# Performance work log

Hardware: AMD Instinct MI355X
Metric: run time of the kernel (lower is better)

Reference implementation:

```python
import jax, jax.numpy as jnp
import numpy as np

D_MODEL, H, D_FF = 1024, 16, 4096
B, S = 2, 2048
EPS = 1e-6


def setup_inputs() -> dict:
    key = jax.random.key(0)
    ks = jax.random.split(key, 12)
    sc = 0.02
    p = lambda k, shape: (jax.random.normal(k, shape, dtype=jnp.float32) * sc)
    return {
        "x": jax.random.normal(ks[0], (B, S, D_MODEL), dtype=jnp.float32),
        "mask": jnp.ones((B, 1, 1, S), dtype=jnp.int32),
        "wq": p(ks[1], (D_MODEL, D_MODEL)), "bq": jnp.zeros((D_MODEL,), jnp.float32),
        "wk": p(ks[2], (D_MODEL, D_MODEL)), "bk": jnp.zeros((D_MODEL,), jnp.float32),
        "wv": p(ks[3], (D_MODEL, D_MODEL)), "bv": jnp.zeros((D_MODEL,), jnp.float32),
        "wo": p(ks[4], (D_MODEL, D_MODEL)), "bo": jnp.zeros((D_MODEL,), jnp.float32),
        "w1": p(ks[5], (D_FF, D_MODEL)), "b1": jnp.zeros((D_FF,), jnp.float32),
        "w2": p(ks[6], (D_MODEL, D_FF)), "b2": jnp.zeros((D_MODEL,), jnp.float32),
        "ln1_a": jnp.ones((D_MODEL,), jnp.float32), "ln1_b": jnp.zeros((D_MODEL,), jnp.float32),
        "ln2_a": jnp.ones((D_MODEL,), jnp.float32), "ln2_b": jnp.zeros((D_MODEL,), jnp.float32),
    }


def _layernorm(x, alpha, beta):
    # Matches the torch module: unbiased std (ddof=1), eps added to std (not var).
    mean = jnp.mean(x, axis=-1, keepdims=True)
    std = jnp.std(x, axis=-1, keepdims=True, ddof=1)
    return alpha * (x - mean) / (std + EPS) + beta


def _mha(x, mask, wq, bq, wk, bk, wv, bv, wo, bo):
    b, s, d = x.shape
    d_k = d // H
    # torch Linear: y = x @ W^T + b
    q = (x @ wq.T + bq).reshape(b, s, H, d_k).transpose(0, 2, 1, 3)
    k = (x @ wk.T + bk).reshape(b, s, H, d_k).transpose(0, 2, 1, 3)
    v = (x @ wv.T + bv).reshape(b, s, H, d_k).transpose(0, 2, 1, 3)
    scores = jnp.einsum("bhqd,bhkd->bhqk", q, k) / jnp.sqrt(jnp.float32(d_k))
    scores = jnp.where(mask == 0, jnp.float32(-1e9), scores)
    attn = jax.nn.softmax(scores, axis=-1)
    out = jnp.einsum("bhqk,bhkd->bhqd", attn, v)
    out = out.transpose(0, 2, 1, 3).reshape(b, s, d)
    return out @ wo.T + bo


def reference(x, mask, wq, bq, wk, bk, wv, bv, wo, bo, w1, b1, w2, b2,
              ln1_a, ln1_b, ln2_a, ln2_b):
    # Pre-LN MHA + residual
    h1 = _layernorm(x, ln1_a, ln1_b)
    x = x + _mha(h1, mask, wq, bq, wk, bk, wv, bv, wo, bo)
    # Pre-LN FFN + residual (dropout=0 -> identity)
    h2 = _layernorm(x, ln2_a, ln2_b)
    ff = jax.nn.relu(h2 @ w1.T + b1) @ w2.T + b2
    return x + ff
```

## Files before the change

kernel.cpp:

```cpp
#include <hip/hip_runtime.h>
#include <cstdint>
#include <cstddef>

typedef short bf16x8 __attribute__((ext_vector_type(8)));
typedef float f32x4 __attribute__((ext_vector_type(4)));

#define D_MODEL 1024
#define SEQ     2048
#define NBATCH  2
#define NH      16
#define DKH     64
#define DFF     4096
#define MROWS   (NBATCH * SEQ)

__device__ __forceinline__ unsigned short f2bf(float f) {
  unsigned u = __builtin_bit_cast(unsigned, f);
  u += 0x7fffu + ((u >> 16) & 1u);
  return (unsigned short)(u >> 16);
}
__device__ __forceinline__ unsigned packbf2(float lo, float hi) {
  unsigned r;
  asm("v_cvt_pk_bf16_f32 %0, %1, %2" : "=v"(r) : "v"(lo), "v"(hi));
  return r;
}
__device__ __forceinline__ void gload_lds16(const void* g, void* l) {
  __builtin_amdgcn_global_load_lds(
      (const __attribute__((address_space(1))) unsigned*)g,
      (__attribute__((address_space(3))) unsigned*)l, 16, 0, 0);
}

__global__ __launch_bounds__(256) void cast_weights_kernel(
    const float* __restrict__ wq, const float* __restrict__ wk,
    const float* __restrict__ wv, const float* __restrict__ wo,
    const float* __restrict__ w1, const float* __restrict__ w2,
    unsigned short* __restrict__ dst) {
  const int TOT4 = (12 << 20) >> 2;
  for (int i4 = blockIdx.x * blockDim.x + threadIdx.x; i4 < TOT4;
       i4 += gridDim.x * blockDim.x) {
    int i = i4 << 2;
    const float* src;
    int off;
    if (i < (4 << 20)) {
      src = (i < (2 << 20)) ? ((i < (1 << 20)) ? wq : wk)
                            : ((i < (3 << 20)) ? wv : wo);
      off = i & ((1 << 20) - 1);
    } else if (i < (8 << 20)) { src = w1; off = i - (4 << 20); }
    else                      { src = w2; off = i - (8 << 20); }
    float4 v = *(const float4*)(src + off);
    ushort4 o;
    o.x = f2bf(v.x); o.y = f2bf(v.y); o.z = f2bf(v.z); o.w = f2bf(v.w);
    *(ushort4*)(dst + i) = o;
  }
}

__global__ __launch_bounds__(256) void ln_kernel(
    const float* __restrict__ x, const float* __restrict__ alpha,
    const float* __restrict__ beta, unsigned short* __restrict__ out) {
  const int row = blockIdx.x;
  const int t = threadIdx.x;
  float4 v = *(const float4*)(x + (size_t)row * D_MODEL + t * 4);
  float s = v.x + v.y + v.z + v.w;
#pragma unroll
  for (int o = 1; o < 64; o <<= 1) s += __shfl_xor(s, o, 64);
  __shared__ float red[8];
  if ((t & 63) == 0) red[t >> 6] = s;
  __syncthreads();
  float mean = (red[0] + red[1] + red[2] + red[3]) * (1.f / D_MODEL);
  float dx = v.x - mean, dy = v.y - mean, dz = v.z - mean, dw = v.w - mean;
  float sq = dx * dx + dy * dy + dz * dz + dw * dw;
#pragma unroll
  for (int o = 1; o < 64; o <<= 1) sq += __shfl_xor(sq, o, 64);
  if ((t & 63) == 0) red[4 + (t >> 6)] = sq;
  __syncthreads();
  float var = (red[4] + red[5] + red[6] + red[7]) * (1.f / (D_MODEL - 1));
  float inv = 1.f / (sqrtf(var) + 1e-6f);
  float4 a = *(const float4*)(alpha + t * 4);
  float4 be = *(const float4*)(beta + t * 4);
  ushort4 o4;
  o4.x = f2bf(a.x * dx * inv + be.x);
  o4.y = f2bf(a.y * dy * inv + be.y);
  o4.z = f2bf(a.z * dz * inv + be.z);
  o4.w = f2bf(a.w * dw * inv + be.w);
  *(ushort4*)(out + (size_t)row * D_MODEL + t * 4) = o4;
}

#define GEMM_STAGE(A_, W_, LD_, koff_, kt_, buf_)                                  \
  {                                                                                \
    int ke_ = (koff_) + (kt_) * 32;                                                \
    gload_lds16(A_ + (size_t)(m0 + srow) * (LD_) + ke_ + sce, &lds[(buf_)][0][t * 8]);        \
    gload_lds16(A_ + (size_t)(m0 + 64 + srow) * (LD_) + ke_ + sce, &lds[(buf_)][0][2048 + t * 8]); \
    gload_lds16(W_ + (size_t)(n0 + srow) * (LD_) + ke_ + sce, &lds[(buf_)][1][t * 8]);        \
    gload_lds16(W_ + (size_t)(n0 + 64 + srow) * (LD_) + ke_ + sce, &lds[(buf_)][1][2048 + t * 8]); \
  }

#define GEMM_MAINLOOP(A_, W_, LD_, K_, koff_)                                      \
  GEMM_STAGE(A_, W_, LD_, koff_, 0, 0);                                            \
  for (int kt = 0; kt < ((K_) >> 5); ++kt) {                                       \
    __syncthreads();                                                               \
    if (kt + 1 < ((K_) >> 5)) GEMM_STAGE(A_, W_, LD_, koff_, kt + 1, (kt + 1) & 1); \
    const unsigned short* la = lds[kt & 1][0];                                     \
    const unsigned short* lb = lds[kt & 1][1];                                     \
    bf16x8 af[4], bfr[4];                                                          \
    _Pragma("unroll") for (int i = 0; i < 4; i++) {                                \
      af[i]  = *(const bf16x8*)&la[(wm + i * 16 + c) * 32 + g * 8];                \
      bfr[i] = *(const bf16x8*)&lb[(wn + i * 16 + c) * 32 + g * 8];                \
    }                                                                              \
    _Pragma("unroll") for (int mi = 0; mi < 4; mi++)                               \
      _Pragma("unroll") for (int ni = 0; ni < 4; ni++)                             \
        acc[mi][ni] = __builtin_amdgcn_mfma_f32_16x16x32_bf16(af[mi], bfr[ni],     \
                                                              acc[mi][ni], 0, 0, 0); \
  }

enum { MODE_BF16 = 0, MODE_RELU = 2, MODE_PARTIAL = 4 };

template <int MODE>
__global__ __launch_bounds__(256) void gemm_bt(
    const unsigned short* __restrict__ A, const unsigned short* __restrict__ W,
    const float* __restrict__ bias, void* __restrict__ outp, int M, int N, int K) {
  __shared__ unsigned short lds[2][2][128 * 32];
  const int t = threadIdx.x;
  const int lane = t & 63, wid = t >> 6;
  const int g = lane >> 4, c = lane & 15;
  const int m0 = blockIdx.y * 128, n0 = blockIdx.x * 128;
  const int wm = (wid >> 1) * 64, wn = (wid & 1) * 64;
  const int srow = t >> 2, sce = (t & 3) * 8;
  const int ldk = K * gridDim.z;
  const int koff = blockIdx.z * K;

  f32x4 zero = {0.f, 0.f, 0.f, 0.f};
  f32x4 acc[4][4];
#pragma unroll
  for (int i = 0; i < 4; i++)
#pragma unroll
    for (int j = 0; j < 4; j++) acc[i][j] = zero;

  GEMM_MAINLOOP(A, W, ldk, K, koff);

  float bv[4];
#pragma unroll
  for (int ni = 0; ni < 4; ni++)
    bv[ni] = (MODE == MODE_PARTIAL) ? 0.f : bias[n0 + wn + ni * 16 + c];

  float* po = (MODE == MODE_PARTIAL)
                  ? ((float*)outp + (size_t)blockIdx.z * M * N) : (float*)outp;

#pragma unroll
  for (int mi = 0; mi < 4; mi++) {
#pragma unroll
    for (int ni = 0; ni < 4; ni++) {
      const int mb = m0 + wm + mi * 16 + g * 4;
      const int n = n0 + wn + ni * 16 + c;
#pragma unroll
      for (int r = 0; r < 4; r++) {
        const int m = mb + r;
        float v = acc[mi][ni][r] + bv[ni];
        if (MODE == MODE_RELU) v = fmaxf(v, 0.f);
        if (MODE == MODE_PARTIAL) {
          po[(size_t)m * N + n] = v;
        } else {
          ((unsigned short*)outp)[(size_t)m * N + n] = f2bf(v);
        }
      }
    }
  }
}

__global__ __launch_bounds__(256) void gemm_qkv(
    const unsigned short* __restrict__ A, const unsigned short* __restrict__ Wbase,
    const float* __restrict__ bq, const float* __restrict__ bk,
    const float* __restrict__ bv_, unsigned short* __restrict__ qkout,
    unsigned short* __restrict__ vtout) {
  __shared__ unsigned short lds[2][2][128 * 32];
  const int t = threadIdx.x;
  const int lane = t & 63, wid = t >> 6;
  const int g = lane >> 4, c = lane & 15;
  const int wsel = blockIdx.x >> 3;
  const int m0 = blockIdx.y * 128, n0 = (blockIdx.x & 7) * 128;
  const int wm = (wid >> 1) * 64, wn = (wid & 1) * 64;
  const int srow = t >> 2, sce = (t & 3) * 8;
  const unsigned short* W = Wbase + ((size_t)wsel << 20);
  const float* bias = (wsel == 0) ? bq : (wsel == 1) ? bk : bv_;

  f32x4 zero = {0.f, 0.f, 0.f, 0.f};
  f32x4 acc[4][4];
#pragma unroll
  for (int i = 0; i < 4; i++)
#pragma unroll
    for (int j = 0; j < 4; j++) acc[i][j] = zero;

  GEMM_MAINLOOP(A, W, 1024, 1024, 0);

  float bvv[4];
#pragma unroll
  for (int ni = 0; ni < 4; ni++) bvv[ni] = bias[n0 + wn + ni * 16 + c];
  const float qsc = (wsel == 0) ? 0.125f : 1.f;

  if (wsel < 2) {
    unsigned short* outp = qkout + ((size_t)wsel << 22);
#pragma unroll
    for (int mi = 0; mi < 4; mi++) {
#pragma unroll
      for (int ni = 0; ni < 4; ni++) {
        const int mb = m0 + wm + mi * 16 + g * 4;
        const int n = n0 + wn + ni * 16 + c;
#pragma unroll
        for (int r = 0; r < 4; r++)
          outp[(size_t)(mb + r) * 1024 + n] = f2bf((acc[mi][ni][r] + bvv[ni]) * qsc);
      }
    }
  } else {
#pragma unroll
    for (int mi = 0; mi < 4; mi++) {
#pragma unroll
      for (int ni = 0; ni < 4; ni++) {
        const int mb = m0 + wm + mi * 16 + g * 4;
        const int n = n0 + wn + ni * 16 + c;
        const int b = mb >> 11, s2 = mb & 2047;
        ushort4 o4;
        o4.x = f2bf(acc[mi][ni][0] + bvv[ni]);
        o4.y = f2bf(acc[mi][ni][1] + bvv[ni]);
        o4.z = f2bf(acc[mi][ni][2] + bvv[ni]);
        o4.w = f2bf(acc[mi][ni][3] + bvv[ni]);
        *(ushort4*)(vtout + ((size_t)(b * 1024 + n)) * 2048 + s2) = o4;
      }
    }
  }
}

#define ATTN_STAGE(base_, buf_)                                                    \
  {                                                                                \
    gload_lds16(Kb + (size_t)((base_) + kr) * D_MODEL + ((kc ^ (kr & 7)) << 3),    \
                &Klds[buf_][t * 8]);                                               \
    gload_lds16(Vb + (size_t)vr * SEQ + (base_) + ((vc2 ^ (vr & 3)) << 3),         \
                &Vlds[buf_][t * 8]);                                               \
  }

__global__ __launch_bounds__(256, 4) void attn_kernel(
    const unsigned short* __restrict__ Q, const unsigned short* __restrict__ Kmat,
    const unsigned short* __restrict__ Vt, const int* __restrict__ mask,
    unsigned short* __restrict__ O) {
  __shared__ unsigned short Klds[2][32 * 64];
  __shared__ unsigned short Vlds[2][64 * 32];
  const int t = threadIdx.x, lane = t & 63, wid = t >> 6;
  const int g = lane >> 4, c = lane & 15;
  const int qt = blockIdx.x, bh = blockIdx.y;
  const int b = bh >> 4, h = bh & 15;
  const int q0 = qt * 64 + wid * 16;

  const unsigned short* Qb = Q + (size_t)b * SEQ * D_MODEL + h * DKH;
  const unsigned short* Kb = Kmat + (size_t)b * SEQ * D_MODEL + h * DKH;
  const unsigned short* Vb = Vt + (size_t)bh * DKH * SEQ;
  const int* mb = mask + b * SEQ;

  const int kr = t >> 3, kc = t & 7;
  const int vr = t >> 2, vc2 = t & 3;

  bf16x8 qf[2];
#pragma unroll
  for (int kd = 0; kd < 2; kd++)
    qf[kd] = *(const bf16x8*)&Qb[(size_t)(q0 + c) * D_MODEL + kd * 32 + g * 8];

  f32x4 zero = {0.f, 0.f, 0.f, 0.f};
  f32x4 of[4];
#pragma unroll
  for (int j = 0; j < 4; j++) of[j] = zero;
  float mrun = -1e30f, lrun = 0.f;

  ATTN_STAGE(0, 0);

  for (int kv = 0; kv < 64; ++kv) {
    const int buf = kv & 1;
    const int base = kv * 32;
    __syncthreads();
    if (kv < 63) ATTN_STAGE(base + 32, buf ^ 1);

    bf16x8 kf[4];
#pragma unroll
    for (int nb = 0; nb < 2; nb++)
#pragma unroll
      for (int kd = 0; kd < 2; kd++)
        kf[nb * 2 + kd] = *(const bf16x8*)&Klds[buf][(nb * 16 + c) * 64 +
                                                     (((kd * 4 + g) ^ (c & 7)) << 3)];
    bf16x8 vf[4];
#pragma unroll
    for (int dkb = 0; dkb < 4; dkb++)
      vf[dkb] = *(const bf16x8*)&Vlds[buf][(dkb * 16 + c) * 32 +
                                           ((g ^ (c & 3)) << 3)];

    int4 mk0 = *(const int4*)&mb[base + g * 4];
    int4 mk1 = *(const int4*)&mb[base + 16 + g * 4];

    f32x4 sf[2];
#pragma unroll
    for (int nb = 0; nb < 2; nb++) {
      f32x4 s = zero;
      s = __builtin_amdgcn_mfma_f32_16x16x32_bf16(kf[nb * 2 + 0], qf[0], s, 0, 0, 0);
      s = __builtin_amdgcn_mfma_f32_16x16x32_bf16(kf[nb * 2 + 1], qf[1], s, 0, 0, 0);
      sf[nb] = s;
    }

    sf[0][0] += (mk0.x == 0) ? -1e9f : 0.f;
    sf[0][1] += (mk0.y == 0) ? -1e9f : 0.f;
    sf[0][2] += (mk0.z == 0) ? -1e9f : 0.f;
    sf[0][3] += (mk0.w == 0) ? -1e9f : 0.f;
    sf[1][0] += (mk1.x == 0) ? -1e9f : 0.f;
    sf[1][1] += (mk1.y == 0) ? -1e9f : 0.f;
    sf[1][2] += (mk1.z == 0) ? -1e9f : 0.f;
    sf[1][3] += (mk1.w == 0) ? -1e9f : 0.f;

    float pm = fmaxf(fmaxf(fmaxf(sf[0][0], sf[0][1]), fmaxf(sf[0][2], sf[0][3])),
                     fmaxf(fmaxf(sf[1][0], sf[1][1]), fmaxf(sf[1][2], sf[1][3])));
    pm = fmaxf(pm, __shfl_xor(pm, 16, 64));
    pm = fmaxf(pm, __shfl_xor(pm, 32, 64));
    if (!__all(pm <= mrun + 8.f)) {
      float mnew = fmaxf(mrun, pm);
      float fsc = exp2f((mrun - mnew) * 1.44269504f);
      lrun *= fsc;
#pragma unroll
      for (int dkb = 0; dkb < 4; dkb++) of[dkb] *= fsc;
      mrun = mnew;
    }
    const float mb2 = mrun * 1.44269504f;
    float ps = 0.f;
#pragma unroll
    for (int nb = 0; nb < 2; nb++)
#pragma unroll
      for (int r = 0; r < 4; r++) {
        float p = exp2f(fmaf(sf[nb][r], 1.44269504f, -mb2));
        sf[nb][r] = p;
        ps += p;
      }
    lrun += ps;

    unsigned pk00 = packbf2(sf[0][0], sf[0][1]);
    unsigned pk01 = packbf2(sf[0][2], sf[0][3]);
    unsigned pk10 = packbf2(sf[1][0], sf[1][1]);
    unsigned pk11 = packbf2(sf[1][2], sf[1][3]);
    const int la = ((g & 1) << 5) + c;
    const int lb2 = la + 16;
    unsigned a00 = __shfl(pk00, la, 64), a01 = __shfl(pk01, la, 64);
    unsigned a10 = __shfl(pk10, la, 64), a11 = __shfl(pk11, la, 64);
    unsigned b00 = __shfl(pk00, lb2, 64), b01 = __shfl(pk01, lb2, 64);
    unsigned b10 = __shfl(pk10, lb2, 64), b11 = __shfl(pk11, lb2, 64);
    const bool hi2 = (g >= 2);
    uint4 pw;
    pw.x = hi2 ? a10 : a00;
    pw.y = hi2 ? a11 : a01;
    pw.z = hi2 ? b10 : b00;
    pw.w = hi2 ? b11 : b01;
    bf16x8 pf = __builtin_bit_cast(bf16x8, pw);
#pragma unroll
    for (int dkb = 0; dkb < 4; dkb++)
      of[dkb] = __builtin_amdgcn_mfma_f32_16x16x32_bf16(vf[dkb], pf, of[dkb], 0, 0, 0);
  }

  float lt = lrun;
  lt += __shfl_xor(lt, 16, 64);
  lt += __shfl_xor(lt, 32, 64);
  float inv = 1.f / lt;
#pragma unroll
  for (int dkb = 0; dkb < 4; dkb++) {
    ushort4 o4;
    o4.x = f2bf(of[dkb][0] * inv);
    o4.y = f2bf(of[dkb][1] * inv);
    o4.z = f2bf(of[dkb][2] * inv);
    o4.w = f2bf(of[dkb][3] * inv);
    *(ushort4*)&O[(size_t)(b * SEQ + q0 + c) * D_MODEL + h * DKH + dkb * 16 +
                  g * 4] = o4;
  }
}

__global__ __launch_bounds__(256) void proj_ln2_kernel(
    const float* __restrict__ x, const float* __restrict__ P0,
    const float* __restrict__ P1, const float* __restrict__ bo,
    const float* __restrict__ alpha, const float* __restrict__ beta,
    float* __restrict__ x2, unsigned short* __restrict__ h2) {
  const int row = blockIdx.x;
  const int t = threadIdx.x;
  const size_t idx = (size_t)row * D_MODEL + t * 4;
  float4 xv = *(const float4*)(x + idx);
  float4 p0 = *(const float4*)(P0 + idx);
  float4 p1 = *(const float4*)(P1 + idx);
  float4 bo4 = *(const float4*)(bo + t * 4);
  float4 v;
  v.x = xv.x + p0.x + p1.x + bo4.x;
  v.y = xv.y + p0.y + p1.y + bo4.y;
  v.z = xv.z + p0.z + p1.z + bo4.z;
  v.w = xv.w + p0.w + p1.w + bo4.w;
  *(float4*)(x2 + idx) = v;

  float s = v.x + v.y + v.z + v.w;
#pragma unroll
  for (int o = 1; o < 64; o <<= 1) s += __shfl_xor(s, o, 64);
  __shared__ float red[8];
  if ((t & 63) == 0) red[t >> 6] = s;
  __syncthreads();
  float mean = (red[0] + red[1] + red[2] + red[3]) * (1.f / D_MODEL);
  float dx = v.x - mean, dy = v.y - mean, dz = v.z - mean, dw = v.w - mean;
  float sq = dx * dx + dy * dy + dz * dz + dw * dw;
#pragma unroll
  for (int o = 1; o < 64; o <<= 1) sq += __shfl_xor(sq, o, 64);
  if ((t & 63) == 0) red[4 + (t >> 6)] = sq;
  __syncthreads();
  float var = (red[4] + red[5] + red[6] + red[7]) * (1.f / (D_MODEL - 1));
  float inv = 1.f / (sqrtf(var) + 1e-6f);
  float4 a = *(const float4*)(alpha + t * 4);
  float4 be = *(const float4*)(beta + t * 4);
  ushort4 o4;
  o4.x = f2bf(a.x * dx * inv + be.x);
  o4.y = f2bf(a.y * dy * inv + be.y);
  o4.z = f2bf(a.z * dz * inv + be.z);
  o4.w = f2bf(a.w * dw * inv + be.w);
  *(ushort4*)(h2 + idx) = o4;
}

__global__ __launch_bounds__(256) void ffn2_add_kernel(
    const float* __restrict__ x2, const float* __restrict__ Q0,
    const float* __restrict__ Q1, const float* __restrict__ b2,
    float* __restrict__ out) {
  const int i4 = blockIdx.x * blockDim.x + threadIdx.x;
  const size_t idx = (size_t)i4 * 4;
  float4 a = *(const float4*)(x2 + idx);
  float4 q0 = *(const float4*)(Q0 + idx);
  float4 q1 = *(const float4*)(Q1 + idx);
  float4 b = *(const float4*)(b2 + ((i4 & 255) * 4));
  float4 v;
  v.x = a.x + q0.x + q1.x + b.x;
  v.y = a.y + q0.y + q1.y + b.y;
  v.z = a.z + q0.z + q1.z + b.z;
  v.w = a.w + q0.w + q1.w + b.w;
  *(float4*)(out + idx) = v;
}

extern "C" void kernel_launch(void* const* d_in, const int* in_sizes, int n_in,
                              void* d_out, int out_size, void* d_ws, size_t ws_size,
                              hipStream_t stream) {
  (void)in_sizes; (void)n_in; (void)out_size; (void)ws_size;
  const float* x    = (const float*)d_in[0];
  const int*   mask = (const int*)d_in[1];
  const float* wq   = (const float*)d_in[2];
  const float* bq   = (const float*)d_in[3];
  const float* wk   = (const float*)d_in[4];
  const float* bk   = (const float*)d_in[5];
  const float* wv   = (const float*)d_in[6];
  const float* bv   = (const float*)d_in[7];
  const float* wo   = (const float*)d_in[8];
  const float* bo   = (const float*)d_in[9];
  const float* w1   = (const float*)d_in[10];
  const float* b1   = (const float*)d_in[11];
  const float* w2   = (const float*)d_in[12];
  const float* b2   = (const float*)d_in[13];
  const float* ln1a = (const float*)d_in[14];
  const float* ln1b = (const float*)d_in[15];
  const float* ln2a = (const float*)d_in[16];
  const float* ln2b = (const float*)d_in[17];

  char* ws = (char*)d_ws;
  unsigned short* w_bf  = (unsigned short*)ws;
  unsigned short* wq_bf = w_bf;
  unsigned short* wo_bf = w_bf + (3u << 20);
  unsigned short* w1_bf = w_bf + (4u << 20);
  unsigned short* w2_bf = w_bf + (8u << 20);
  unsigned short* h1    = (unsigned short*)(ws + (24u << 20));
  unsigned short* qbuf  = (unsigned short*)(ws + (32u << 20));
  unsigned short* kbuf  = (unsigned short*)(ws + (40u << 20));
  unsigned short* vtbuf = (unsigned short*)(ws + (48u << 20));
  unsigned short* attnb = (unsigned short*)(ws + (56u << 20));
  float*          x2    = (float*)(ws + (64u << 20));
  unsigned short* h2    = (unsigned short*)(ws + (80u << 20));
  unsigned short* ffn1  = (unsigned short*)(ws + (88u << 20));
  float*          pp    = (float*)(ws + (88u << 20));
  float*          qq    = (float*)(ws + (24u << 20));

  cast_weights_kernel<<<1024, 256, 0, stream>>>(wq, wk, wv, wo, w1, w2, w_bf);
  ln_kernel<<<MROWS, 256, 0, stream>>>(x, ln1a, ln1b, h1);
  gemm_qkv<<<dim3(24, 32), 256, 0, stream>>>(h1, wq_bf, bq, bk, bv, qbuf, vtbuf);
  attn_kernel<<<dim3(32, 32), 256, 0, stream>>>(qbuf, kbuf, vtbuf, mask, attnb);
  gemm_bt<MODE_PARTIAL><<<dim3(8, 32, 2), 256, 0, stream>>>(
      attnb, wo_bf, nullptr, (void*)pp, MROWS, D_MODEL, 512);
  proj_ln2_kernel<<<MROWS, 256, 0, stream>>>(
      x, pp, pp + (size_t)MROWS * D_MODEL, bo, ln2a, ln2b, x2, h2);
  gemm_bt<MODE_RELU><<<dim3(32, 32), 256, 0, stream>>>(
      h2, w1_bf, b1, (void*)ffn1, MROWS, DFF, D_MODEL);
  gemm_bt<MODE_PARTIAL><<<dim3(8, 32, 2), 256, 0, stream>>>(
      ffn1, w2_bf, nullptr, (void*)qq, MROWS, D_MODEL, 2048);
  ffn2_add_kernel<<<4096, 256, 0, stream>>>(
      x2, qq, qq + (size_t)MROWS * D_MODEL, b2, (float*)d_out);
}
```

Baseline: 297.3 us.

## Shrink attention blocks to two waves and use 16x16x16 MFMA for PV

The attention kernel now runs 128-thread blocks covering 32 query rows, doubling the grid, and each thread issues two LDS-direct loads per K and V tile. The PV product uses 16x16x16 bf16 MFMAs fed directly from the softmax registers, which removes the cross-lane shuffles that repacked P for the 16x16x32 instruction. The int mask is precomputed into an additive float bias inside the weight-cast kernel, so the inner loop adds it instead of doing compares. In exchange, the smaller blocks mean each K/V tile is loaded into LDS by more blocks, and the PV step issues twice as many smaller MFMAs.

```diff
diff --git a/kernel.cpp b/kernel.cpp
--- a/kernel.cpp
+++ b/kernel.cpp
@@ -3,6 +3,7 @@
 #include <cstddef>
 
 typedef short bf16x8 __attribute__((ext_vector_type(8)));
+typedef short bf16x4 __attribute__((ext_vector_type(4)));
 typedef float f32x4 __attribute__((ext_vector_type(4)));
 
 #define D_MODEL 1024
@@ -13,6 +14,16 @@
 #define DFF     4096
 #define MROWS   (NBATCH * SEQ)
 
+#if __has_builtin(__builtin_amdgcn_mfma_f32_16x16x16bf16_1k)
+#define HAVE_MFMA16 1
+#define MFMA16(a, b, c) __builtin_amdgcn_mfma_f32_16x16x16bf16_1k(a, b, c, 0, 0, 0)
+#elif __has_builtin(__builtin_amdgcn_mfma_f32_16x16x16_bf16)
+#define HAVE_MFMA16 1
+#define MFMA16(a, b, c) __builtin_amdgcn_mfma_f32_16x16x16_bf16(a, b, c, 0, 0, 0)
+#else
+#define HAVE_MFMA16 0
+#endif
+
 __device__ __forceinline__ unsigned short f2bf(float f) {
   unsigned u = __builtin_bit_cast(unsigned, f);
   u += 0x7fffu + ((u >> 16) & 1u);
@@ -33,10 +44,11 @@
     const float* __restrict__ wq, const float* __restrict__ wk,
     const float* __restrict__ wv, const float* __restrict__ wo,
     const float* __restrict__ w1, const float* __restrict__ w2,
-    unsigned short* __restrict__ dst) {
+    const int* __restrict__ mask, unsigned short* __restrict__ dst,
+    float* __restrict__ maskf) {
   const int TOT4 = (12 << 20) >> 2;
-  for (int i4 = blockIdx.x * blockDim.x + threadIdx.x; i4 < TOT4;
-       i4 += gridDim.x * blockDim.x) {
+  const int gid = blockIdx.x * blockDim.x + threadIdx.x;
+  for (int i4 = gid; i4 < TOT4; i4 += gridDim.x * blockDim.x) {
     int i = i4 << 2;
     const float* src;
     int off;
@@ -50,6 +62,15 @@
     ushort4 o;
     o.x = f2bf(v.x); o.y = f2bf(v.y); o.z = f2bf(v.z); o.w = f2bf(v.w);
     *(ushort4*)(dst + i) = o;
+  }
+  if (gid < (NBATCH * SEQ / 4)) {
+    int4 m = ((const int4*)mask)[gid];
+    float4 f;
+    f.x = (m.x == 0) ? -1e9f : 0.f;
+    f.y = (m.y == 0) ? -1e9f : 0.f;
+    f.z = (m.z == 0) ? -1e9f : 0.f;
+    f.w = (m.w == 0) ? -1e9f : 0.f;
+    ((float4*)maskf)[gid] = f;
   }
 }
 
@@ -227,17 +248,22 @@
   }
 }
 
-#define ATTN_STAGE(base_, buf_)                                                    \
-  {                                                                                \
-    gload_lds16(Kb + (size_t)((base_) + kr) * D_MODEL + ((kc ^ (kr & 7)) << 3),    \
-                &Klds[buf_][t * 8]);                                               \
-    gload_lds16(Vb + (size_t)vr * SEQ + (base_) + ((vc2 ^ (vr & 3)) << 3),         \
-                &Vlds[buf_][t * 8]);                                               \
-  }
-
-__global__ __launch_bounds__(256, 4) void attn_kernel(
+#define ATTN_STAGE(base_, buf_)                                                     \
+  {                                                                                 \
+    const int i0 = t, i1 = t + 128;                                                 \
+    gload_lds16(Kb + (size_t)((base_) + (i0 >> 3)) * D_MODEL +                      \
+                    (((i0 & 7) ^ ((i0 >> 3) & 7)) << 3), &Klds[buf_][i0 * 8]);      \
+    gload_lds16(Kb + (size_t)((base_) + (i1 >> 3)) * D_MODEL +                      \
+                    (((i1 & 7) ^ ((i1 >> 3) & 7)) << 3), &Klds[buf_][i1 * 8]);      \
+    gload_lds16(Vb + (size_t)(i0 >> 2) * SEQ + (base_) +                            \
+                    (((i0 & 3) ^ ((i0 >> 2) & 3)) << 3), &Vlds[buf_][i0 * 8]);      \
+    gload_lds16(Vb + (size_t)(i1 >> 2) * SEQ + (base_) +                            \
+                    (((i1 & 3) ^ ((i1 >> 2) & 3)) << 3), &Vlds[buf_][i1 * 8]);      \
+  }
+
+__global__ __launch_bounds__(128, 4) void attn_kernel(
     const unsigned short* __restrict__ Q, const unsigned short* __restrict__ Kmat,
-    const unsigned short* __restrict__ Vt, const int* __restrict__ mask,
+    const unsigned short* __restrict__ Vt, const float* __restrict__ maskf,
     unsigned short* __restrict__ O) {
   __shared__ unsigned short Klds[2][32 * 64];
   __shared__ unsigned short Vlds[2][64 * 32];
@@ -245,15 +271,12 @@
   const int g = lane >> 4, c = lane & 15;
   const int qt = blockIdx.x, bh = blockIdx.y;
   const int b = bh >> 4, h = bh & 15;
-  const int q0 = qt * 64 + wid * 16;
+  const int q0 = qt * 32 + wid * 16;
 
   const unsigned short* Qb = Q + (size_t)b * SEQ * D_MODEL + h * DKH;
   const unsigned short* Kb = Kmat + (size_t)b * SEQ * D_MODEL + h * DKH;
   const unsigned short* Vb = Vt + (size_t)bh * DKH * SEQ;
-  const int* mb = mask + b * SEQ;
-
-  const int kr = t >> 3, kc = t & 7;
-  const int vr = t >> 2, vc2 = t & 3;
+  const float* mbf = maskf + b * SEQ;
 
   bf16x8 qf[2];
 #pragma unroll
@@ -281,14 +304,27 @@
       for (int kd = 0; kd < 2; kd++)
         kf[nb * 2 + kd] = *(const bf16x8*)&Klds[buf][(nb * 16 + c) * 64 +
                                                      (((kd * 4 + g) ^ (c & 7)) << 3)];
+#if HAVE_MFMA16
+    bf16x4 vv[2][4];
+#pragma unroll
+    for (int nb = 0; nb < 2; nb++)
+#pragma unroll
+      for (int dkb = 0; dkb < 4; dkb++) {
+        const int vrow = dkb * 16 + c;
+        const int vbyte = vrow * 64 + ((((nb << 1) + (g >> 1)) ^ (c & 3)) << 4) +
+                          ((g & 1) << 3);
+        vv[nb][dkb] = *(const bf16x4*)((const char*)Vlds[buf] + vbyte);
+      }
+#else
     bf16x8 vf[4];
 #pragma unroll
     for (int dkb = 0; dkb < 4; dkb++)
       vf[dkb] = *(const bf16x8*)&Vlds[buf][(dkb * 16 + c) * 32 +
                                            ((g ^ (c & 3)) << 3)];
-
-    int4 mk0 = *(const int4*)&mb[base + g * 4];
-    int4 mk1 = *(const int4*)&mb[base + 16 + g * 4];
+#endif
+
+    float4 ma0 = *(const float4*)&mbf[base + g * 4];
+    float4 ma1 = *(const float4*)&mbf[base + 16 + g * 4];
 
     f32x4 sf[2];
 #pragma unroll
@@ -299,14 +335,8 @@
       sf[nb] = s;
     }
 
-    sf[0][0] += (mk0.x == 0) ? -1e9f : 0.f;
-    sf[0][1] += (mk0.y == 0) ? -1e9f : 0.f;
-    sf[0][2] += (mk0.z == 0) ? -1e9f : 0.f;
-    sf[0][3] += (mk0.w == 0) ? -1e9f : 0.f;
-    sf[1][0] += (mk1.x == 0) ? -1e9f : 0.f;
-    sf[1][1] += (mk1.y == 0) ? -1e9f : 0.f;
-    sf[1][2] += (mk1.z == 0) ? -1e9f : 0.f;
-    sf[1][3] += (mk1.w == 0) ? -1e9f : 0.f;
+    sf[0][0] += ma0.x; sf[0][1] += ma0.y; sf[0][2] += ma0.z; sf[0][3] += ma0.w;
+    sf[1][0] += ma1.x; sf[1][1] += ma1.y; sf[1][2] += ma1.z; sf[1][3] += ma1.w;
 
     float pm = fmaxf(fmaxf(fmaxf(sf[0][0], sf[0][1]), fmaxf(sf[0][2], sf[0][3])),
                      fmaxf(fmaxf(sf[1][0], sf[1][1]), fmaxf(sf[1][2], sf[1][3])));
@@ -332,6 +362,19 @@
       }
     lrun += ps;
 
+#if HAVE_MFMA16
+#pragma unroll
+    for (int nb = 0; nb < 2; nb++) {
+      unsigned plo = packbf2(sf[nb][0], sf[nb][1]);
+      unsigned phi = packbf2(sf[nb][2], sf[nb][3]);
+      unsigned long long uu = (unsigned long long)plo |
+                              ((unsigned long long)phi << 32);
+      bf16x4 pf = __builtin_bit_cast(bf16x4, uu);
+#pragma unroll
+      for (int dkb = 0; dkb < 4; dkb++)
+        of[dkb] = MFMA16(vv[nb][dkb], pf, of[dkb]);
+    }
+#else
     unsigned pk00 = packbf2(sf[0][0], sf[0][1]);
     unsigned pk01 = packbf2(sf[0][2], sf[0][3]);
     unsigned pk10 = packbf2(sf[1][0], sf[1][1]);
@@ -352,6 +395,7 @@
 #pragma unroll
     for (int dkb = 0; dkb < 4; dkb++)
       of[dkb] = __builtin_amdgcn_mfma_f32_16x16x32_bf16(vf[dkb], pf, of[dkb], 0, 0, 0);
+#endif
   }
 
   float lt = lrun;
@@ -471,11 +515,13 @@
   unsigned short* ffn1  = (unsigned short*)(ws + (88u << 20));
   float*          pp    = (float*)(ws + (88u << 20));
   float*          qq    = (float*)(ws + (24u << 20));
-
-  cast_weights_kernel<<<1024, 256, 0, stream>>>(wq, wk, wv, wo, w1, w2, w_bf);
+  float*          maskf = (float*)(ws + (120u << 20));
+
+  cast_weights_kernel<<<1024, 256, 0, stream>>>(wq, wk, wv, wo, w1, w2, mask,
+                                                w_bf, maskf);
   ln_kernel<<<MROWS, 256, 0, stream>>>(x, ln1a, ln1b, h1);
   gemm_qkv<<<dim3(24, 32), 256, 0, stream>>>(h1, wq_bf, bq, bk, bv, qbuf, vtbuf);
-  attn_kernel<<<dim3(32, 32), 256, 0, stream>>>(qbuf, kbuf, vtbuf, mask, attnb);
+  attn_kernel<<<dim3(64, 32), 128, 0, stream>>>(qbuf, kbuf, vtbuf, maskf, attnb);
   gemm_bt<MODE_PARTIAL><<<dim3(8, 32, 2), 256, 0, stream>>>(
       attnb, wo_bf, nullptr, (void*)pp, MROWS, D_MODEL, 512);
   proj_ln2_kernel<<<MROWS, 256, 0, stream>>>(
```

New measurement: 295.9 us. Within noise of the previous version (-0.5%).
